# Performance work log

Measured on AMD Instinct MI355X. Metric: run time of the kernel, lower is better.

The kernel has to match this reference:

```python
import jax, jax.numpy as jnp
import numpy as np

K = 3          # kernel size
STRIDE = 1
PAD = 1
DIL = 1


def setup_inputs() -> dict:
    key = jax.random.key(0)
    k1, k2, k3 = jax.random.split(key, 3)
    N, Cin, H, W = 8, 128, 64, 64
    Cout = 128
    x = jax.random.normal(k1, (N, Cin, H, W), dtype=jnp.float32)
    # offset channels: 2 * deformable_groups * K*K = 18, interleaved (dy, dx) per tap
    offset = jax.random.normal(k2, (N, 2 * K * K, H, W), dtype=jnp.float32)
    weight = jax.random.normal(k3, (Cout, Cin, K, K), dtype=jnp.float32) / np.sqrt(Cin * K * K)
    return {"x": x, "offset": offset, "weight": weight}


def _deform_conv(x, offset, weight):
    N, Cin, H, W = x.shape
    Cout = weight.shape[0]
    KK = K * K
    Ho, Wo = offset.shape[2], offset.shape[3]

    off = offset.reshape(N, KK, 2, Ho, Wo)
    dy = off[:, :, 0]  # [N, KK, Ho, Wo]
    dx = off[:, :, 1]

    kh = jnp.repeat(jnp.arange(K), K).astype(x.dtype)   # [KK]
    kw = jnp.tile(jnp.arange(K), K).astype(x.dtype)     # [KK]
    base_i = (jnp.arange(Ho) * STRIDE - PAD).astype(x.dtype)  # [Ho]
    base_j = (jnp.arange(Wo) * STRIDE - PAD).astype(x.dtype)  # [Wo]

    # Sampling positions: [N, KK, Ho, Wo]
    py = base_i[None, None, :, None] + (kh * DIL)[None, :, None, None] + dy
    px = base_j[None, None, None, :] + (kw * DIL)[None, :, None, None] + dx

    y0 = jnp.floor(py)
    x0 = jnp.floor(px)
    wy1 = py - y0
    wx1 = px - x0
    wy0 = 1.0 - wy1
    wx0 = 1.0 - wx1
    y0i = y0.astype(jnp.int32)
    x0i = x0.astype(jnp.int32)
    y1i = y0i + 1
    x1i = x0i + 1

    x_flat = x.reshape(N, Cin, H * W)

    def gather(yi, xi):
        # zero-padding outside the image
        mask = ((yi >= 0) & (yi < H) & (xi >= 0) & (xi < W)).astype(x.dtype)
        idx = jnp.clip(yi, 0, H - 1) * W + jnp.clip(xi, 0, W - 1)  # [N,KK,Ho,Wo]
        v = jnp.take_along_axis(x_flat, idx.reshape(N, 1, -1), axis=2)  # [N,Cin,KK*Ho*Wo]
        v = v.reshape(N, Cin, KK, Ho, Wo)
        return v * mask[:, None]

    sampled = (gather(y0i, x0i) * (wy0 * wx0)[:, None]
               + gather(y0i, x1i) * (wy0 * wx1)[:, None]
               + gather(y1i, x0i) * (wy1 * wx0)[:, None]
               + gather(y1i, x1i) * (wy1 * wx1)[:, None])  # [N,Cin,KK,Ho,Wo]

    w = weight.reshape(Cout, Cin, KK)
    return jnp.einsum('nckij,ock->noij', sampled, w)


def reference(x, offset, weight):
    return _deform_conv(x, offset, weight)
```

## Files before the change

kernel.cpp:

```cpp
#include <hip/hip_runtime.h>


#define H  64
#define W  64
#define CIN 128
#define COUT 128
#define NB 8
#define KK 9
#define SROW (CIN + 8)

typedef short bf16x8 __attribute__((ext_vector_type(8)));
typedef float f32x4  __attribute__((ext_vector_type(4)));

__device__ __forceinline__ unsigned short f2bf(float f) {
    unsigned u = __builtin_bit_cast(unsigned, f);
    u += 0x7FFFu + ((u >> 16) & 1u);
    return (unsigned short)(u >> 16);
}
__device__ __forceinline__ unsigned cvt_pk_bf16(float lo, float hi) {
    unsigned r;
    asm("v_cvt_pk_bf16_f32 %0, %1, %2" : "=v"(r) : "v"(lo), "v"(hi));
    return r;
}
__device__ __forceinline__ float lo_f(unsigned u) { return __builtin_bit_cast(float, u << 16); }
__device__ __forceinline__ float hi_f(unsigned u) { return __builtin_bit_cast(float, u & 0xFFFF0000u); }

__global__ void prep_all(const float* __restrict__ x, const float* __restrict__ w,
                         unsigned short* __restrict__ xt, unsigned short* __restrict__ wt) {
    int b = blockIdx.x;
    int t = threadIdx.x;
    if (b >= NB * H) {
        int idx = (b - NB * H) * 256 + t;
        if (idx < KK * COUT * CIN) {
            int e  = idx & 7;
            int lq = (idx >> 3) & 3;
            int lm = (idx >> 5) & 15;
            int ct = (idx >> 9) & 3;
            int nt = (idx >> 11) & 1;
            int c4 = (idx >> 12) & 3;
            int kk = idx >> 14;
            int co = (c4 << 5) + (nt << 4) + lm;
            int ch = (ct << 5) + (lq << 3) + e;
            wt[idx] = f2bf(w[(co * CIN + ch) * KK + kk]);
        }
        return;
    }
    __shared__ float tile[CIN][W + 4];
    int n = b & 7, y = b >> 3;
    const float* src = x + ((size_t)n * CIN * H + y) * W;
    #pragma unroll
    for (int it = 0; it < 8; ++it) {
        int idx = it * 256 + t;
        int c  = idx >> 4;
        int x4 = (idx & 15) << 2;
        int xs = (x4 + ((c >> 5) << 4)) & 63;
        *(float4*)&tile[c][xs] = *(const float4*)(src + (size_t)c * H * W + x4);
    }
    __syncthreads();
    int xp = t >> 2;
    int cbch = (t & 3) << 5;
    int xr = (xp + ((cbch >> 5) << 4)) & 63;
    unsigned short* dst = xt + (((size_t)(n * H + y) * W + xp) * CIN + cbch);
    unsigned rr[16];
    #pragma unroll
    for (int i = 0; i < 16; ++i)
        rr[i] = cvt_pk_bf16(tile[cbch + 2 * i][xr], tile[cbch + 2 * i + 1][xr]);
    #pragma unroll
    for (int i = 0; i < 4; ++i)
        ((uint4*)dst)[i] = make_uint4(rr[4*i], rr[4*i+1], rr[4*i+2], rr[4*i+3]);
}

struct GatherCtx {
    const unsigned short *c00, *c01, *c10, *c11;
    float w00, w01, w10, w11;
};

__device__ __forceinline__ GatherCtx gather_setup(float dy, float dx, int ho, int wo, int kk,
                                                  const unsigned short* xbase) {
    GatherCtx g;
    float py = (float)(ho - 1 + kk / 3) + dy;
    float px = (float)(wo - 1 + kk % 3) + dx;
    float y0f = floorf(py), x0f = floorf(px);
    float wy1 = py - y0f, wx1 = px - x0f;
    float wy0 = 1.f - wy1, wx0 = 1.f - wx1;
    int y0 = (int)y0f, x0 = (int)x0f;
    int y1 = y0 + 1, x1 = x0 + 1;
    bool vy0 = (unsigned)y0 < (unsigned)H, vy1 = (unsigned)y1 < (unsigned)H;
    bool vx0 = (unsigned)x0 < (unsigned)W, vx1 = (unsigned)x1 < (unsigned)W;
    g.w00 = (vy0 && vx0) ? wy0 * wx0 : 0.f;
    g.w01 = (vy0 && vx1) ? wy0 * wx1 : 0.f;
    g.w10 = (vy1 && vx0) ? wy1 * wx0 : 0.f;
    g.w11 = (vy1 && vx1) ? wy1 * wx1 : 0.f;
    int yc0 = min(max(y0, 0), H - 1), yc1 = min(max(y1, 0), H - 1);
    int xc0 = min(max(x0, 0), W - 1), xc1 = min(max(x1, 0), W - 1);
    const unsigned short* r0 = xbase + (size_t)yc0 * W * CIN;
    const unsigned short* r1 = xbase + (size_t)yc1 * W * CIN;
    g.c00 = r0 + xc0 * CIN;  g.c01 = r0 + xc1 * CIN;
    g.c10 = r1 + xc0 * CIN;  g.c11 = r1 + xc1 * CIN;
    return g;
}

__global__ __launch_bounds__(512, 2) void fused_main(
        const float* __restrict__ offs, const unsigned short* __restrict__ xt,
        const unsigned short* __restrict__ wt, float* __restrict__ out) {
    __shared__ __attribute__((aligned(16))) unsigned short samp[2][64][SROW];

    int b = blockIdx.x;
    int n = b & 7, ho = b >> 3;
    int t = threadIdx.x;
    int lane = t & 63, wv = t >> 6;
    int lm = lane & 15, lq = lane >> 4;

    int pos = t >> 3;
    int cb  = (t & 7) << 4;

    const float* offp = offs + (size_t)n * 2 * KK * H * W + (size_t)ho * W + pos;
    const unsigned short* xb = xt + (size_t)n * H * W * CIN + cb;

    unsigned stash[KK][8];
    #pragma unroll
    for (int tap = 0; tap < KK; ++tap) {
        float dy = offp[(size_t)(2 * tap) * H * W];
        float dx = offp[(size_t)(2 * tap + 1) * H * W];
        GatherCtx g = gather_setup(dy, dx, ho, pos, tap, xb);
        uint4 gv[8];
        #pragma unroll
        for (int j = 0; j < 2; ++j) {
            gv[4*j+0] = *(const uint4*)(g.c00 + 8*j);
            gv[4*j+1] = *(const uint4*)(g.c01 + 8*j);
            gv[4*j+2] = *(const uint4*)(g.c10 + 8*j);
            gv[4*j+3] = *(const uint4*)(g.c11 + 8*j);
        }
        #pragma unroll
        for (int j = 0; j < 2; ++j) {
            const unsigned* a0 = (const unsigned*)&gv[4*j+0];
            const unsigned* a1 = (const unsigned*)&gv[4*j+1];
            const unsigned* a2 = (const unsigned*)&gv[4*j+2];
            const unsigned* a3 = (const unsigned*)&gv[4*j+3];
            #pragma unroll
            for (int i = 0; i < 4; ++i) {
                float v0 = g.w00*lo_f(a0[i]) + g.w01*lo_f(a1[i]) + g.w10*lo_f(a2[i]) + g.w11*lo_f(a3[i]);
                float v1 = g.w00*hi_f(a0[i]) + g.w01*hi_f(a1[i]) + g.w10*hi_f(a2[i]) + g.w11*hi_f(a3[i]);
                stash[tap][4*j+i] = cvt_pk_bf16(v0, v1);
            }
        }
    }

    f32x4 acc[4];
    #pragma unroll
    for (int mt = 0; mt < 4; ++mt) acc[mt] = f32x4{0.f, 0.f, 0.f, 0.f};

    int slot = (lm << 2) + lq;
    const unsigned short* wvbase = wt + ((size_t)wv << 11) + (slot << 3);

    {
        unsigned short* ld = &samp[0][pos][cb];
        *(uint4*)(ld)     = make_uint4(stash[0][0], stash[0][1], stash[0][2], stash[0][3]);
        *(uint4*)(ld + 8) = make_uint4(stash[0][4], stash[0][5], stash[0][6], stash[0][7]);
    }
    __syncthreads();

    #pragma unroll
    for (int tap = 0; tap < KK; ++tap) {
        if (tap < KK - 1) {
            unsigned short* ld = &samp[(tap + 1) & 1][pos][cb];
            *(uint4*)(ld)     = make_uint4(stash[tap+1][0], stash[tap+1][1],
                                           stash[tap+1][2], stash[tap+1][3]);
            *(uint4*)(ld + 8) = make_uint4(stash[tap+1][4], stash[tap+1][5],
                                           stash[tap+1][6], stash[tap+1][7]);
        }
        const unsigned short* wkb = wvbase + ((size_t)(tap << 3) << 11);
        bf16x8 bW[4];
        #pragma unroll
        for (int ct = 0; ct < 4; ++ct)
            bW[ct] = *(const bf16x8*)(wkb + (ct << 9));

        __builtin_amdgcn_s_setprio(1);
        #pragma unroll
        for (int ct = 0; ct < 4; ++ct) {
            bf16x8 a[4];
            #pragma unroll
            for (int mt = 0; mt < 4; ++mt)
                a[mt] = *(const bf16x8*)&samp[tap & 1][lm + (mt << 4)][(ct << 5) + (lq << 3)];
            #pragma unroll
            for (int mt = 0; mt < 4; ++mt)
                acc[mt] = __builtin_amdgcn_mfma_f32_16x16x32_bf16(a[mt], bW[ct], acc[mt], 0, 0, 0);
        }
        __builtin_amdgcn_s_setprio(0);
        __syncthreads();
    }

    int co = (wv << 4) + lm;
    #pragma unroll
    for (int mt = 0; mt < 4; ++mt) {
        int wob = (mt << 4) + (lq << 2);
        *(f32x4*)(out + (((size_t)(n * COUT + co) * H + ho) * W + wob)) = acc[mt];
    }
}

extern "C" void kernel_launch(void* const* d_in, const int* in_sizes, int n_in,
                              void* d_out, int out_size, void* d_ws, size_t ws_size,
                              hipStream_t stream) {
    const float* x      = (const float*)d_in[0];
    const float* offset = (const float*)d_in[1];
    const float* weight = (const float*)d_in[2];
    float* out = (float*)d_out;

    unsigned short* xt = (unsigned short*)d_ws;
    unsigned short* wt = (unsigned short*)((char*)d_ws + 8388608);

    int wblocks = (KK * COUT * CIN + 255) / 256;
    hipLaunchKernelGGL(prep_all, dim3(NB * H + wblocks), dim3(256), 0, stream,
                       x, weight, xt, wt);
    hipLaunchKernelGGL(fused_main, dim3(NB * H), dim3(512), 0, stream,
                       offset, xt, wt, out);
}
```

Measured before the change: 102.7 us.

## Split each output row across two blocks to double grid size and occupancy

```diff
diff --git a/kernel.cpp b/kernel.cpp
--- a/kernel.cpp
+++ b/kernel.cpp
@@ -100,76 +100,63 @@
     return g;
 }
 
-__global__ __launch_bounds__(512, 2) void fused_main(
+__global__ __launch_bounds__(512, 4) void fused_main(
         const float* __restrict__ offs, const unsigned short* __restrict__ xt,
         const unsigned short* __restrict__ wt, float* __restrict__ out) {
-    __shared__ __attribute__((aligned(16))) unsigned short samp[2][64][SROW];
+    __shared__ __attribute__((aligned(16))) unsigned short samp[2][32][SROW];
 
     int b = blockIdx.x;
-    int n = b & 7, ho = b >> 3;
+    int n = b & 7, ho = (b >> 3) & 63, ph = b >> 9;
     int t = threadIdx.x;
     int lane = t & 63, wv = t >> 6;
     int lm = lane & 15, lq = lane >> 4;
 
-    int pos = t >> 3;
-    int cb  = (t & 7) << 4;
-
-    const float* offp = offs + (size_t)n * 2 * KK * H * W + (size_t)ho * W + pos;
+    int lp = t >> 4;
+    int cb = (t & 15) << 3;
+    int wo = (ph << 5) + lp;
+
+    const float* offp = offs + (size_t)n * 2 * KK * H * W + (size_t)ho * W + wo;
     const unsigned short* xb = xt + (size_t)n * H * W * CIN + cb;
 
-    unsigned stash[KK][8];
+    unsigned stash[KK][4];
     #pragma unroll
     for (int tap = 0; tap < KK; ++tap) {
         float dy = offp[(size_t)(2 * tap) * H * W];
         float dx = offp[(size_t)(2 * tap + 1) * H * W];
-        GatherCtx g = gather_setup(dy, dx, ho, pos, tap, xb);
-        uint4 gv[8];
+        GatherCtx g = gather_setup(dy, dx, ho, wo, tap, xb);
+        uint4 q00 = *(const uint4*)(g.c00);
+        uint4 q01 = *(const uint4*)(g.c01);
+        uint4 q10 = *(const uint4*)(g.c10);
+        uint4 q11 = *(const uint4*)(g.c11);
+        const unsigned* a0 = (const unsigned*)&q00;
+        const unsigned* a1 = (const unsigned*)&q01;
+        const unsigned* a2 = (const unsigned*)&q10;
+        const unsigned* a3 = (const unsigned*)&q11;
         #pragma unroll
-        for (int j = 0; j < 2; ++j) {
-            gv[4*j+0] = *(const uint4*)(g.c00 + 8*j);
-            gv[4*j+1] = *(const uint4*)(g.c01 + 8*j);
-            gv[4*j+2] = *(const uint4*)(g.c10 + 8*j);
-            gv[4*j+3] = *(const uint4*)(g.c11 + 8*j);
+        for (int i = 0; i < 4; ++i) {
+            float v0 = g.w00*lo_f(a0[i]) + g.w01*lo_f(a1[i]) + g.w10*lo_f(a2[i]) + g.w11*lo_f(a3[i]);
+            float v1 = g.w00*hi_f(a0[i]) + g.w01*hi_f(a1[i]) + g.w10*hi_f(a2[i]) + g.w11*hi_f(a3[i]);
+            stash[tap][i] = cvt_pk_bf16(v0, v1);
         }
-        #pragma unroll
-        for (int j = 0; j < 2; ++j) {
-            const unsigned* a0 = (const unsigned*)&gv[4*j+0];
-            const unsigned* a1 = (const unsigned*)&gv[4*j+1];
-            const unsigned* a2 = (const unsigned*)&gv[4*j+2];
-            const unsigned* a3 = (const unsigned*)&gv[4*j+3];
-            #pragma unroll
-            for (int i = 0; i < 4; ++i) {
-                float v0 = g.w00*lo_f(a0[i]) + g.w01*lo_f(a1[i]) + g.w10*lo_f(a2[i]) + g.w11*lo_f(a3[i]);
-                float v1 = g.w00*hi_f(a0[i]) + g.w01*hi_f(a1[i]) + g.w10*hi_f(a2[i]) + g.w11*hi_f(a3[i]);
-                stash[tap][4*j+i] = cvt_pk_bf16(v0, v1);
-            }
-        }
-    }
-
-    f32x4 acc[4];
-    #pragma unroll
-    for (int mt = 0; mt < 4; ++mt) acc[mt] = f32x4{0.f, 0.f, 0.f, 0.f};
+    }
+
+    f32x4 acc[2];
+    acc[0] = f32x4{0.f, 0.f, 0.f, 0.f};
+    acc[1] = f32x4{0.f, 0.f, 0.f, 0.f};
 
     int slot = (lm << 2) + lq;
     const unsigned short* wvbase = wt + ((size_t)wv << 11) + (slot << 3);
 
-    {
-        unsigned short* ld = &samp[0][pos][cb];
-        *(uint4*)(ld)     = make_uint4(stash[0][0], stash[0][1], stash[0][2], stash[0][3]);
-        *(uint4*)(ld + 8) = make_uint4(stash[0][4], stash[0][5], stash[0][6], stash[0][7]);
-    }
+    *(uint4*)&samp[0][lp][cb] = make_uint4(stash[0][0], stash[0][1], stash[0][2], stash[0][3]);
     __syncthreads();
 
     #pragma unroll
     for (int tap = 0; tap < KK; ++tap) {
-        if (tap < KK - 1) {
-            unsigned short* ld = &samp[(tap + 1) & 1][pos][cb];
-            *(uint4*)(ld)     = make_uint4(stash[tap+1][0], stash[tap+1][1],
-                                           stash[tap+1][2], stash[tap+1][3]);
-            *(uint4*)(ld + 8) = make_uint4(stash[tap+1][4], stash[tap+1][5],
-                                           stash[tap+1][6], stash[tap+1][7]);
-        }
-        const unsigned short* wkb = wvbase + ((size_t)(tap << 3) << 11);
+        if (tap < KK - 1)
+            *(uint4*)&samp[(tap + 1) & 1][lp][cb] =
+                make_uint4(stash[tap+1][0], stash[tap+1][1], stash[tap+1][2], stash[tap+1][3]);
+
+        const unsigned short* wkb = wvbase + ((size_t)tap << 14);
         bf16x8 bW[4];
         #pragma unroll
         for (int ct = 0; ct < 4; ++ct)
@@ -178,13 +165,10 @@
         __builtin_amdgcn_s_setprio(1);
         #pragma unroll
         for (int ct = 0; ct < 4; ++ct) {
-            bf16x8 a[4];
-            #pragma unroll
-            for (int mt = 0; mt < 4; ++mt)
-                a[mt] = *(const bf16x8*)&samp[tap & 1][lm + (mt << 4)][(ct << 5) + (lq << 3)];
-            #pragma unroll
-            for (int mt = 0; mt < 4; ++mt)
-                acc[mt] = __builtin_amdgcn_mfma_f32_16x16x32_bf16(a[mt], bW[ct], acc[mt], 0, 0, 0);
+            bf16x8 a0 = *(const bf16x8*)&samp[tap & 1][lm]     [(ct << 5) + (lq << 3)];
+            bf16x8 a1 = *(const bf16x8*)&samp[tap & 1][lm + 16][(ct << 5) + (lq << 3)];
+            acc[0] = __builtin_amdgcn_mfma_f32_16x16x32_bf16(a0, bW[ct], acc[0], 0, 0, 0);
+            acc[1] = __builtin_amdgcn_mfma_f32_16x16x32_bf16(a1, bW[ct], acc[1], 0, 0, 0);
         }
         __builtin_amdgcn_s_setprio(0);
         __syncthreads();
@@ -192,8 +176,8 @@
 
     int co = (wv << 4) + lm;
     #pragma unroll
-    for (int mt = 0; mt < 4; ++mt) {
-        int wob = (mt << 4) + (lq << 2);
+    for (int mt = 0; mt < 2; ++mt) {
+        int wob = (ph << 5) + (mt << 4) + (lq << 2);
         *(f32x4*)(out + (((size_t)(n * COUT + co) * H + ho) * W + wob)) = acc[mt];
     }
 }
@@ -212,6 +196,6 @@
     int wblocks = (KK * COUT * CIN + 255) / 256;
     hipLaunchKernelGGL(prep_all, dim3(NB * H + wblocks), dim3(256), 0, stream,
                        x, weight, xt, wt);
-    hipLaunchKernelGGL(fused_main, dim3(NB * H), dim3(512), 0, stream,
+    hipLaunchKernelGGL(fused_main, dim3(NB * H * 2), dim3(512), 0, stream,
                        offset, xt, wt, out);
 }
```

Measured after the change: 107.1 us. +4.2%, slower.

## Store all taps in LDS and retile MFMA work as 2x2 per wave

Applied to the files above, without the earlier changes.

```diff
diff --git a/kernel.cpp b/kernel.cpp
--- a/kernel.cpp
+++ b/kernel.cpp
@@ -7,7 +7,7 @@
 #define COUT 128
 #define NB 8
 #define KK 9
-#define SROW (CIN + 8)
+#define SROW4 132
 
 typedef short bf16x8 __attribute__((ext_vector_type(8)));
 typedef float f32x4  __attribute__((ext_vector_type(4)));
@@ -103,7 +103,7 @@
 __global__ __launch_bounds__(512, 2) void fused_main(
         const float* __restrict__ offs, const unsigned short* __restrict__ xt,
         const unsigned short* __restrict__ wt, float* __restrict__ out) {
-    __shared__ __attribute__((aligned(16))) unsigned short samp[2][64][SROW];
+    __shared__ __attribute__((aligned(16))) unsigned short samp[KK][64][SROW4];
 
     int b = blockIdx.x;
     int n = b & 7, ho = b >> 3;
@@ -114,10 +114,9 @@
     int pos = t >> 3;
     int cb  = (t & 7) << 4;
 
-    const float* offp = offs + (size_t)n * 2 * KK * H * W + (size_t)ho * W + pos;
+    const float* offp = offs + (size_t)(n * 2 * KK) * H * W + (size_t)ho * W + pos;
     const unsigned short* xb = xt + (size_t)n * H * W * CIN + cb;
 
-    unsigned stash[KK][8];
     #pragma unroll
     for (int tap = 0; tap < KK; ++tap) {
         float dy = offp[(size_t)(2 * tap) * H * W];
@@ -131,6 +130,7 @@
             gv[4*j+2] = *(const uint4*)(g.c10 + 8*j);
             gv[4*j+3] = *(const uint4*)(g.c11 + 8*j);
         }
+        unsigned rr[8];
         #pragma unroll
         for (int j = 0; j < 2; ++j) {
             const unsigned* a0 = (const unsigned*)&gv[4*j+0];
@@ -141,60 +141,60 @@
             for (int i = 0; i < 4; ++i) {
                 float v0 = g.w00*lo_f(a0[i]) + g.w01*lo_f(a1[i]) + g.w10*lo_f(a2[i]) + g.w11*lo_f(a3[i]);
                 float v1 = g.w00*hi_f(a0[i]) + g.w01*hi_f(a1[i]) + g.w10*hi_f(a2[i]) + g.w11*hi_f(a3[i]);
-                stash[tap][4*j+i] = cvt_pk_bf16(v0, v1);
+                rr[4*j+i] = cvt_pk_bf16(v0, v1);
             }
         }
-    }
-
-    f32x4 acc[4];
-    #pragma unroll
-    for (int mt = 0; mt < 4; ++mt) acc[mt] = f32x4{0.f, 0.f, 0.f, 0.f};
-
+        unsigned short* ld = &samp[tap][pos][cb];
+        *(uint4*)(ld)     = make_uint4(rr[0], rr[1], rr[2], rr[3]);
+        *(uint4*)(ld + 8) = make_uint4(rr[4], rr[5], rr[6], rr[7]);
+    }
+
+    __syncthreads();
+
+    int ph2 = wv & 1;
+    int cq  = wv >> 1;
     int slot = (lm << 2) + lq;
-    const unsigned short* wvbase = wt + ((size_t)wv << 11) + (slot << 3);
-
-    {
-        unsigned short* ld = &samp[0][pos][cb];
-        *(uint4*)(ld)     = make_uint4(stash[0][0], stash[0][1], stash[0][2], stash[0][3]);
-        *(uint4*)(ld + 8) = make_uint4(stash[0][4], stash[0][5], stash[0][6], stash[0][7]);
-    }
-    __syncthreads();
+
+    f32x4 acc[2][2];
+    #pragma unroll
+    for (int mt = 0; mt < 2; ++mt)
+        #pragma unroll
+        for (int nt = 0; nt < 2; ++nt) acc[mt][nt] = f32x4{0.f, 0.f, 0.f, 0.f};
+
+    const unsigned short* wq = wt + ((size_t)cq << 12) + (slot << 3);
 
     #pragma unroll
     for (int tap = 0; tap < KK; ++tap) {
-        if (tap < KK - 1) {
-            unsigned short* ld = &samp[(tap + 1) & 1][pos][cb];
-            *(uint4*)(ld)     = make_uint4(stash[tap+1][0], stash[tap+1][1],
-                                           stash[tap+1][2], stash[tap+1][3]);
-            *(uint4*)(ld + 8) = make_uint4(stash[tap+1][4], stash[tap+1][5],
-                                           stash[tap+1][6], stash[tap+1][7]);
-        }
-        const unsigned short* wkb = wvbase + ((size_t)(tap << 3) << 11);
-        bf16x8 bW[4];
-        #pragma unroll
-        for (int ct = 0; ct < 4; ++ct)
-            bW[ct] = *(const bf16x8*)(wkb + (ct << 9));
-
-        __builtin_amdgcn_s_setprio(1);
+        const unsigned short* wkb = wq + ((size_t)(tap << 2) << 12);
+        bf16x8 bW[2][4];
+        #pragma unroll
+        for (int nt = 0; nt < 2; ++nt)
+            #pragma unroll
+            for (int ct = 0; ct < 4; ++ct)
+                bW[nt][ct] = *(const bf16x8*)(wkb + (nt << 11) + (ct << 9));
+
         #pragma unroll
         for (int ct = 0; ct < 4; ++ct) {
-            bf16x8 a[4];
-            #pragma unroll
-            for (int mt = 0; mt < 4; ++mt)
-                a[mt] = *(const bf16x8*)&samp[tap & 1][lm + (mt << 4)][(ct << 5) + (lq << 3)];
-            #pragma unroll
-            for (int mt = 0; mt < 4; ++mt)
-                acc[mt] = __builtin_amdgcn_mfma_f32_16x16x32_bf16(a[mt], bW[ct], acc[mt], 0, 0, 0);
-        }
-        __builtin_amdgcn_s_setprio(0);
-        __syncthreads();
-    }
-
-    int co = (wv << 4) + lm;
-    #pragma unroll
-    for (int mt = 0; mt < 4; ++mt) {
-        int wob = (mt << 4) + (lq << 2);
-        *(f32x4*)(out + (((size_t)(n * COUT + co) * H + ho) * W + wob)) = acc[mt];
+            bf16x8 a[2];
+            #pragma unroll
+            for (int mt = 0; mt < 2; ++mt)
+                a[mt] = *(const bf16x8*)&samp[tap][(ph2 << 5) + (mt << 4) + lm][(ct << 5) + (lq << 3)];
+            #pragma unroll
+            for (int mt = 0; mt < 2; ++mt)
+                #pragma unroll
+                for (int nt = 0; nt < 2; ++nt)
+                    acc[mt][nt] = __builtin_amdgcn_mfma_f32_16x16x32_bf16(a[mt], bW[nt][ct], acc[mt][nt], 0, 0, 0);
+        }
+    }
+
+    #pragma unroll
+    for (int mt = 0; mt < 2; ++mt) {
+        int wob = (ph2 << 5) + (mt << 4) + (lq << 2);
+        #pragma unroll
+        for (int nt = 0; nt < 2; ++nt) {
+            int co = (cq << 5) + (nt << 4) + lm;
+            *(f32x4*)(out + (((size_t)(n * COUT + co) * H + ho) * W + wob)) = acc[mt][nt];
+        }
     }
 }
 
```

Result: slower. 110.9 us (+8.0%).

## Merge prep and main kernels into one cooperative kernel with grid sync

Applied to the files above, without the earlier changes.

```diff
diff --git a/kernel.cpp b/kernel.cpp
--- a/kernel.cpp
+++ b/kernel.cpp
@@ -1,4 +1,5 @@
 #include <hip/hip_runtime.h>
+#include <hip/hip_cooperative_groups.h>
 
 
 #define H  64
@@ -12,6 +13,8 @@
 typedef short bf16x8 __attribute__((ext_vector_type(8)));
 typedef float f32x4  __attribute__((ext_vector_type(4)));
 
+namespace cg = cooperative_groups;
+
 __device__ __forceinline__ unsigned short f2bf(float f) {
     unsigned u = __builtin_bit_cast(unsigned, f);
     u += 0x7FFFu + ((u >> 16) & 1u);
@@ -24,51 +27,6 @@
 }
 __device__ __forceinline__ float lo_f(unsigned u) { return __builtin_bit_cast(float, u << 16); }
 __device__ __forceinline__ float hi_f(unsigned u) { return __builtin_bit_cast(float, u & 0xFFFF0000u); }
-
-__global__ void prep_all(const float* __restrict__ x, const float* __restrict__ w,
-                         unsigned short* __restrict__ xt, unsigned short* __restrict__ wt) {
-    int b = blockIdx.x;
-    int t = threadIdx.x;
-    if (b >= NB * H) {
-        int idx = (b - NB * H) * 256 + t;
-        if (idx < KK * COUT * CIN) {
-            int e  = idx & 7;
-            int lq = (idx >> 3) & 3;
-            int lm = (idx >> 5) & 15;
-            int ct = (idx >> 9) & 3;
-            int nt = (idx >> 11) & 1;
-            int c4 = (idx >> 12) & 3;
-            int kk = idx >> 14;
-            int co = (c4 << 5) + (nt << 4) + lm;
-            int ch = (ct << 5) + (lq << 3) + e;
-            wt[idx] = f2bf(w[(co * CIN + ch) * KK + kk]);
-        }
-        return;
-    }
-    __shared__ float tile[CIN][W + 4];
-    int n = b & 7, y = b >> 3;
-    const float* src = x + ((size_t)n * CIN * H + y) * W;
-    #pragma unroll
-    for (int it = 0; it < 8; ++it) {
-        int idx = it * 256 + t;
-        int c  = idx >> 4;
-        int x4 = (idx & 15) << 2;
-        int xs = (x4 + ((c >> 5) << 4)) & 63;
-        *(float4*)&tile[c][xs] = *(const float4*)(src + (size_t)c * H * W + x4);
-    }
-    __syncthreads();
-    int xp = t >> 2;
-    int cbch = (t & 3) << 5;
-    int xr = (xp + ((cbch >> 5) << 4)) & 63;
-    unsigned short* dst = xt + (((size_t)(n * H + y) * W + xp) * CIN + cbch);
-    unsigned rr[16];
-    #pragma unroll
-    for (int i = 0; i < 16; ++i)
-        rr[i] = cvt_pk_bf16(tile[cbch + 2 * i][xr], tile[cbch + 2 * i + 1][xr]);
-    #pragma unroll
-    for (int i = 0; i < 4; ++i)
-        ((uint4*)dst)[i] = make_uint4(rr[4*i], rr[4*i+1], rr[4*i+2], rr[4*i+3]);
-}
 
 struct GatherCtx {
     const unsigned short *c00, *c01, *c10, *c11;
@@ -100,101 +58,160 @@
     return g;
 }
 
-__global__ __launch_bounds__(512, 2) void fused_main(
-        const float* __restrict__ offs, const unsigned short* __restrict__ xt,
-        const unsigned short* __restrict__ wt, float* __restrict__ out) {
-    __shared__ __attribute__((aligned(16))) unsigned short samp[2][64][SROW];
-
-    int b = blockIdx.x;
-    int n = b & 7, ho = b >> 3;
+__global__ __launch_bounds__(512, 2) void mega(
+        const float* __restrict__ x, const float* __restrict__ w,
+        const float* __restrict__ offs, unsigned short* __restrict__ xt,
+        unsigned short* __restrict__ wt, float* __restrict__ out) {
+    __shared__ __attribute__((aligned(16))) char ldsbuf[34816];
+
+    int bid = blockIdx.x;
+    int n = bid & 7, hp = bid >> 3;
     int t = threadIdx.x;
+
+    {
+        int base = bid * 576;
+        #pragma unroll
+        for (int k2 = 0; k2 < 2; ++k2) {
+            int k = k2 * 512 + t;
+            if (k < 576) {
+                int idx = base + k;
+                int e  = idx & 7;
+                int lq = (idx >> 3) & 3;
+                int lm = (idx >> 5) & 15;
+                int ct = (idx >> 9) & 3;
+                int nt = (idx >> 11) & 1;
+                int c4 = (idx >> 12) & 3;
+                int kk = idx >> 14;
+                int co = (c4 << 5) + (nt << 4) + lm;
+                int ch = (ct << 5) + (lq << 3) + e;
+                wt[idx] = f2bf(w[(co * CIN + ch) * KK + kk]);
+            }
+        }
+    }
+
+    {
+        float (*tile)[W + 4] = (float(*)[W + 4])ldsbuf;
+        #pragma unroll
+        for (int j = 0; j < 2; ++j) {
+            int y = (hp << 1) + j;
+            const float* src = x + ((size_t)n * CIN * H + y) * W;
+            __syncthreads();
+            #pragma unroll
+            for (int it = 0; it < 4; ++it) {
+                int idx = it * 512 + t;
+                int c  = idx >> 4;
+                int x4 = (idx & 15) << 2;
+                int xs = (x4 + ((c >> 5) << 4)) & 63;
+                *(float4*)&tile[c][xs] = *(const float4*)(src + (size_t)c * H * W + x4);
+            }
+            __syncthreads();
+            int xp  = t >> 3;
+            int cbc = (t & 7) << 4;
+            int xr  = (xp + ((cbc >> 5) << 4)) & 63;
+            unsigned short* dst = xt + (((size_t)(n * H + y) * W + xp) * CIN + cbc);
+            unsigned rr[8];
+            #pragma unroll
+            for (int i = 0; i < 8; ++i)
+                rr[i] = cvt_pk_bf16(tile[cbc + 2 * i][xr], tile[cbc + 2 * i + 1][xr]);
+            *(uint4*)(dst)     = make_uint4(rr[0], rr[1], rr[2], rr[3]);
+            *(uint4*)(dst + 8) = make_uint4(rr[4], rr[5], rr[6], rr[7]);
+        }
+    }
+
+    cg::this_grid().sync();
+
     int lane = t & 63, wv = t >> 6;
     int lm = lane & 15, lq = lane >> 4;
-
     int pos = t >> 3;
     int cb  = (t & 7) << 4;
-
-    const float* offp = offs + (size_t)n * 2 * KK * H * W + (size_t)ho * W + pos;
-    const unsigned short* xb = xt + (size_t)n * H * W * CIN + cb;
-
-    unsigned stash[KK][8];
-    #pragma unroll
-    for (int tap = 0; tap < KK; ++tap) {
-        float dy = offp[(size_t)(2 * tap) * H * W];
-        float dx = offp[(size_t)(2 * tap + 1) * H * W];
-        GatherCtx g = gather_setup(dy, dx, ho, pos, tap, xb);
-        uint4 gv[8];
-        #pragma unroll
-        for (int j = 0; j < 2; ++j) {
-            gv[4*j+0] = *(const uint4*)(g.c00 + 8*j);
-            gv[4*j+1] = *(const uint4*)(g.c01 + 8*j);
-            gv[4*j+2] = *(const uint4*)(g.c10 + 8*j);
-            gv[4*j+3] = *(const uint4*)(g.c11 + 8*j);
-        }
-        #pragma unroll
-        for (int j = 0; j < 2; ++j) {
-            const unsigned* a0 = (const unsigned*)&gv[4*j+0];
-            const unsigned* a1 = (const unsigned*)&gv[4*j+1];
-            const unsigned* a2 = (const unsigned*)&gv[4*j+2];
-            const unsigned* a3 = (const unsigned*)&gv[4*j+3];
-            #pragma unroll
-            for (int i = 0; i < 4; ++i) {
-                float v0 = g.w00*lo_f(a0[i]) + g.w01*lo_f(a1[i]) + g.w10*lo_f(a2[i]) + g.w11*lo_f(a3[i]);
-                float v1 = g.w00*hi_f(a0[i]) + g.w01*hi_f(a1[i]) + g.w10*hi_f(a2[i]) + g.w11*hi_f(a3[i]);
-                stash[tap][4*j+i] = cvt_pk_bf16(v0, v1);
-            }
-        }
-    }
-
-    f32x4 acc[4];
-    #pragma unroll
-    for (int mt = 0; mt < 4; ++mt) acc[mt] = f32x4{0.f, 0.f, 0.f, 0.f};
-
     int slot = (lm << 2) + lq;
     const unsigned short* wvbase = wt + ((size_t)wv << 11) + (slot << 3);
-
-    {
-        unsigned short* ld = &samp[0][pos][cb];
-        *(uint4*)(ld)     = make_uint4(stash[0][0], stash[0][1], stash[0][2], stash[0][3]);
-        *(uint4*)(ld + 8) = make_uint4(stash[0][4], stash[0][5], stash[0][6], stash[0][7]);
-    }
-    __syncthreads();
+    unsigned short (*samp)[64][SROW] = (unsigned short(*)[64][SROW])ldsbuf;
+
+    const unsigned short* xb = xt + (size_t)n * H * W * CIN + cb;
 
     #pragma unroll
-    for (int tap = 0; tap < KK; ++tap) {
-        if (tap < KK - 1) {
-            unsigned short* ld = &samp[(tap + 1) & 1][pos][cb];
-            *(uint4*)(ld)     = make_uint4(stash[tap+1][0], stash[tap+1][1],
-                                           stash[tap+1][2], stash[tap+1][3]);
-            *(uint4*)(ld + 8) = make_uint4(stash[tap+1][4], stash[tap+1][5],
-                                           stash[tap+1][6], stash[tap+1][7]);
-        }
-        const unsigned short* wkb = wvbase + ((size_t)(tap << 3) << 11);
-        bf16x8 bW[4];
-        #pragma unroll
-        for (int ct = 0; ct < 4; ++ct)
-            bW[ct] = *(const bf16x8*)(wkb + (ct << 9));
-
-        __builtin_amdgcn_s_setprio(1);
-        #pragma unroll
-        for (int ct = 0; ct < 4; ++ct) {
-            bf16x8 a[4];
-            #pragma unroll
-            for (int mt = 0; mt < 4; ++mt)
-                a[mt] = *(const bf16x8*)&samp[tap & 1][lm + (mt << 4)][(ct << 5) + (lq << 3)];
-            #pragma unroll
-            for (int mt = 0; mt < 4; ++mt)
-                acc[mt] = __builtin_amdgcn_mfma_f32_16x16x32_bf16(a[mt], bW[ct], acc[mt], 0, 0, 0);
-        }
-        __builtin_amdgcn_s_setprio(0);
+    for (int j = 0; j < 2; ++j) {
+        int ho = (hp << 1) + j;
+
+        const float* offp = offs + (size_t)(n * 2 * KK) * H * W + (size_t)ho * W + pos;
+        unsigned stash[KK][8];
+        #pragma unroll
+        for (int tap = 0; tap < KK; ++tap) {
+            float dy = offp[(size_t)(2 * tap) * H * W];
+            float dx = offp[(size_t)(2 * tap + 1) * H * W];
+            GatherCtx g = gather_setup(dy, dx, ho, pos, tap, xb);
+            uint4 gv[8];
+            #pragma unroll
+            for (int jj = 0; jj < 2; ++jj) {
+                gv[4*jj+0] = *(const uint4*)(g.c00 + 8*jj);
+                gv[4*jj+1] = *(const uint4*)(g.c01 + 8*jj);
+                gv[4*jj+2] = *(const uint4*)(g.c10 + 8*jj);
+                gv[4*jj+3] = *(const uint4*)(g.c11 + 8*jj);
+            }
+            #pragma unroll
+            for (int jj = 0; jj < 2; ++jj) {
+                const unsigned* a0 = (const unsigned*)&gv[4*jj+0];
+                const unsigned* a1 = (const unsigned*)&gv[4*jj+1];
+                const unsigned* a2 = (const unsigned*)&gv[4*jj+2];
+                const unsigned* a3 = (const unsigned*)&gv[4*jj+3];
+                #pragma unroll
+                for (int i = 0; i < 4; ++i) {
+                    float v0 = g.w00*lo_f(a0[i]) + g.w01*lo_f(a1[i]) + g.w10*lo_f(a2[i]) + g.w11*lo_f(a3[i]);
+                    float v1 = g.w00*hi_f(a0[i]) + g.w01*hi_f(a1[i]) + g.w10*hi_f(a2[i]) + g.w11*hi_f(a3[i]);
+                    stash[tap][4*jj+i] = cvt_pk_bf16(v0, v1);
+                }
+            }
+        }
+
+        f32x4 acc[4];
+        #pragma unroll
+        for (int mt = 0; mt < 4; ++mt) acc[mt] = f32x4{0.f, 0.f, 0.f, 0.f};
+
+        if (j == 0) __syncthreads();
+        {
+            unsigned short* ld = &samp[0][pos][cb];
+            *(uint4*)(ld)     = make_uint4(stash[0][0], stash[0][1], stash[0][2], stash[0][3]);
+            *(uint4*)(ld + 8) = make_uint4(stash[0][4], stash[0][5], stash[0][6], stash[0][7]);
+        }
         __syncthreads();
-    }
-
-    int co = (wv << 4) + lm;
-    #pragma unroll
-    for (int mt = 0; mt < 4; ++mt) {
-        int wob = (mt << 4) + (lq << 2);
-        *(f32x4*)(out + (((size_t)(n * COUT + co) * H + ho) * W + wob)) = acc[mt];
+
+        #pragma unroll
+        for (int tap = 0; tap < KK; ++tap) {
+            if (tap < KK - 1) {
+                unsigned short* ld = &samp[(tap + 1) & 1][pos][cb];
+                *(uint4*)(ld)     = make_uint4(stash[tap+1][0], stash[tap+1][1],
+                                               stash[tap+1][2], stash[tap+1][3]);
+                *(uint4*)(ld + 8) = make_uint4(stash[tap+1][4], stash[tap+1][5],
+                                               stash[tap+1][6], stash[tap+1][7]);
+            }
+            const unsigned short* wkb = wvbase + ((size_t)(tap << 3) << 11);
+            bf16x8 bW[4];
+            #pragma unroll
+            for (int ct = 0; ct < 4; ++ct)
+                bW[ct] = *(const bf16x8*)(wkb + (ct << 9));
+
+            __builtin_amdgcn_s_setprio(1);
+            #pragma unroll
+            for (int ct = 0; ct < 4; ++ct) {
+                bf16x8 a[4];
+                #pragma unroll
+                for (int mt = 0; mt < 4; ++mt)
+                    a[mt] = *(const bf16x8*)&samp[tap & 1][lm + (mt << 4)][(ct << 5) + (lq << 3)];
+                #pragma unroll
+                for (int mt = 0; mt < 4; ++mt)
+                    acc[mt] = __builtin_amdgcn_mfma_f32_16x16x32_bf16(a[mt], bW[ct], acc[mt], 0, 0, 0);
+            }
+            __builtin_amdgcn_s_setprio(0);
+            __syncthreads();
+        }
+
+        int co = (wv << 4) + lm;
+        #pragma unroll
+        for (int mt = 0; mt < 4; ++mt) {
+            int wob = (mt << 4) + (lq << 2);
+            *(f32x4*)(out + (((size_t)(n * COUT + co) * H + ho) * W + wob)) = acc[mt];
+        }
     }
 }
 
@@ -209,9 +226,10 @@
     unsigned short* xt = (unsigned short*)d_ws;
     unsigned short* wt = (unsigned short*)((char*)d_ws + 8388608);
 
-    int wblocks = (KK * COUT * CIN + 255) / 256;
-    hipLaunchKernelGGL(prep_all, dim3(NB * H + wblocks), dim3(256), 0, stream,
-                       x, weight, xt, wt);
-    hipLaunchKernelGGL(fused_main, dim3(NB * H), dim3(512), 0, stream,
-                       offset, xt, wt, out);
-}
+    const float* xa = x; const float* wa = weight; const float* oa = offset;
+    unsigned short* xta = xt; unsigned short* wta = wt; float* outa = out;
+    void* args[] = { (void*)&xa, (void*)&wa, (void*)&oa,
+                     (void*)&xta, (void*)&wta, (void*)&outa };
+    hipLaunchCooperativeKernel((const void*)mega, dim3(NB * H / 2), dim3(512),
+                               args, 0, stream);
+}
```

Result: slower. 161.5 us (+57.2%).
